# Optimization experiments

Hardware: AMD Instinct MI355X
Metric: run time of the kernel (lower is better)

Reference implementation:

```python
import jax, jax.numpy as jnp
import numpy as np
import math

B, N, D, H = 16, 1024, 1024, 8
HD = D // H
SCALE = 1.0 / math.sqrt(D // 8)
NEG = -1e30


def setup_inputs() -> dict:
    key = jax.random.key(0)
    ks = jax.random.split(key, 10)
    s = 0.02
    return {
        "x": jax.random.normal(ks[0], (B, N, D), dtype=jnp.float32),
        "x_mask": jax.random.randint(ks[1], (B, N), 0, 2, dtype=jnp.int32),
        "Wq": jax.random.normal(ks[2], (H, D, HD), dtype=jnp.float32) * s,
        "bq": jnp.zeros((H, HD), dtype=jnp.float32),
        "Wk": jax.random.normal(ks[3], (H, D, HD), dtype=jnp.float32) * s,
        "bk": jnp.zeros((H, HD), dtype=jnp.float32),
        "Wv": jax.random.normal(ks[4], (H, D, HD), dtype=jnp.float32) * s,
        "bv": jnp.zeros((H, HD), dtype=jnp.float32),
        "Wfc": jax.random.normal(ks[5], (D, D), dtype=jnp.float32) * s,
        "bfc": jnp.zeros((D,), dtype=jnp.float32),
    }


def reference(x, x_mask, Wq, bq, Wk, bk, Wv, bv, Wfc, bfc):
    # per-head projections, stacked: [B, H, N, HD]
    q = jnp.einsum("bnd,hde->bhne", x, Wq) + bq[None, :, None, :]
    k = jnp.einsum("bnd,hde->bhne", x, Wk) + bk[None, :, None, :]
    v = jnp.einsum("bnd,hde->bhne", x, Wv) + bv[None, :, None, :]
    # pairwise padding mask: mask & mask^T  ->  outer product for 0/1 values
    m = x_mask.astype(x.dtype)  # [B, N]
    mask = m[:, :, None] * m[:, None, :]  # [B, N, N]
    scores = jnp.einsum("bhne,bhme->bhnm", q, k) * SCALE  # [B, H, N, N]
    scores = scores * mask[:, None] + NEG * (1.0 - mask[:, None])
    attn = jax.nn.softmax(scores, axis=-1)
    o = jnp.einsum("bhnm,bhme->bhne", attn, v)  # [B, H, N, HD]
    # concat heads along feature dim (head order preserved)
    o = jnp.transpose(o, (0, 2, 1, 3)).reshape(B, N, D)
    out = o @ Wfc + bfc  # final fc; F.dropout result is discarded in source
    return out
```

## Files before the change

kernel.cpp:

```cpp
#include <hip/hip_runtime.h>
#include <hip/hip_bf16.h>
#include <math.h>

#define BN 1024
#define DD 1024
#define NB 16
#define NH 8
#define HDIM 128

typedef __attribute__((ext_vector_type(8))) short bf16x8;
typedef __attribute__((ext_vector_type(4))) float f32x4;
typedef __attribute__((ext_vector_type(16))) float f32x16;
typedef __attribute__((ext_vector_type(4))) unsigned short ushort4v;

#define DEV __device__ __forceinline__

DEV unsigned short f2bf(float f) {
  unsigned u = __float_as_uint(f);
  u = (u + 0x7fffu + ((u >> 16) & 1u)) >> 16;
  return (unsigned short)u;
}

DEV f32x4 mfma16(bf16x8 a, bf16x8 b, f32x4 c) {
  return __builtin_amdgcn_mfma_f32_16x16x32_bf16(a, b, c, 0, 0, 0);
}

DEV f32x16 mfma32(bf16x8 a, bf16x8 b, f32x16 c) {
  return __builtin_amdgcn_mfma_f32_32x32x16_bf16(a, b, c, 0, 0, 0);
}

DEV void async16(const unsigned short* g, unsigned short* l) {
  __builtin_amdgcn_global_load_lds(
      (const __attribute__((address_space(1))) unsigned short*)g,
      (__attribute__((address_space(3))) unsigned short*)l, 16, 0, 0);
}

DEV unsigned cvtpk(float lo, float hi_) {
  unsigned r;
  asm("v_cvt_pk_bf16_f32 %0, %1, %2" : "=v"(r) : "v"(lo), "v"(hi_));
  return r;
}
DEV void swap32(unsigned& a, unsigned& b) {
  asm volatile("v_permlane32_swap_b32 %0, %1" : "+v"(a), "+v"(b));
}
DEV bf16x8 mk8(unsigned a, unsigned b, unsigned c, unsigned d) {
  union { unsigned u[4]; bf16x8 v; } t;
  t.u[0] = a; t.u[1] = b; t.u[2] = c; t.u[3] = d;
  return t.v;
}

__global__ __launch_bounds__(256) void prep_kernel(
    const float* __restrict__ x, const float* __restrict__ Wq,
    const float* __restrict__ Wk, const float* __restrict__ Wv,
    const float* __restrict__ Wfc, unsigned short* __restrict__ x_bf,
    unsigned short* __restrict__ wqkvT, unsigned short* __restrict__ wfcT) {
  __shared__ float tile[32][33];
  const int bx = blockIdx.x, tid = threadIdx.x;
  if (bx < 16384) {
    int i = bx * 256 + tid;
    const float4* p = (const float4*)x;
    float4 v = p[i];
    ushort4v o;
    o[0] = f2bf(v.x); o[1] = f2bf(v.y); o[2] = f2bf(v.z); o[3] = f2bf(v.w);
    *(ushort4v*)(x_bf + (size_t)i * 4) = o;
    return;
  }
  const int tx = tid & 31, ty = tid >> 5;
  if (bx < 19456) {
    int idx = bx - 16384;
    int k0 = (idx & 31) * 32, e0 = ((idx >> 5) & 3) * 32, z = idx >> 7;
    int which = z >> 3, h = z & 7;
    const float* in = (which == 0 ? Wq : (which == 1 ? Wk : Wv)) + (size_t)h * DD * HDIM;
#pragma unroll
    for (int i = 0; i < 4; ++i)
      tile[ty + i * 8][tx] = in[(size_t)(k0 + ty + i * 8) * HDIM + e0 + tx];
    __syncthreads();
    int rowbase = which * 1024 + h * 128 + e0;
#pragma unroll
    for (int i = 0; i < 4; ++i)
      wqkvT[(size_t)(rowbase + ty + i * 8) * DD + k0 + tx] = f2bf(tile[tx][ty + i * 8]);
  } else {
    int idx = bx - 19456;
    int d0 = (idx & 31) * 32, c0 = (idx >> 5) * 32;
#pragma unroll
    for (int i = 0; i < 4; ++i)
      tile[ty + i * 8][tx] = Wfc[(size_t)(d0 + ty + i * 8) * DD + c0 + tx];
    __syncthreads();
#pragma unroll
    for (int i = 0; i < 4; ++i)
      wfcT[(size_t)(c0 + ty + i * 8) * DD + d0 + tx] = f2bf(tile[tx][ty + i * 8]);
  }
}

template <int MODE>
__global__ __launch_bounds__(256, 3) void gemm128_kernel(
    const unsigned short* __restrict__ A, const unsigned short* __restrict__ Bt,
    const float* __restrict__ bias0, const float* __restrict__ bias1,
    const float* __restrict__ bias2, unsigned short* __restrict__ out0,
    unsigned short* __restrict__ out1, unsigned short* __restrict__ out2,
    float* __restrict__ outf) {
  __shared__ unsigned short as[128 * 64];
  __shared__ unsigned short bs[128 * 64];
  const int tid = threadIdx.x;
  const int wave = tid >> 6, lane = tid & 63, quad = lane >> 4, l15 = lane & 15;
  const int wr = wave >> 1, wc = wave & 1;
  const int m0 = (blockIdx.x & 127) << 7, n0 = (blockIdx.x >> 7) << 7;
  f32x4 acc[4][4] = {};

  const int srow = wave * 32 + (lane >> 3);
  const int gch = ((lane & 7) - (lane >> 3)) & 7;
  const unsigned short* ag = A + (size_t)(m0 + srow) * 1024 + gch * 8;
  const unsigned short* bg = Bt + (size_t)(n0 + srow) * 1024 + gch * 8;
  unsigned short* as_w = as + wave * 32 * 64;
  unsigned short* bs_w = bs + wave * 32 * 64;

  for (int kb = 0; kb < 1024; kb += 64) {
#pragma unroll
    for (int i = 0; i < 4; ++i) {
      async16(ag + kb + i * 8 * 1024, as_w + i * 512);
      async16(bg + kb + i * 8 * 1024, bs_w + i * 512);
    }
    __syncthreads();
#pragma unroll
    for (int ks = 0; ks < 2; ++ks) {
      const int sl = ((quad + ks * 4 + l15) & 7) * 8;
      bf16x8 af[4], bfr[4];
#pragma unroll
      for (int mt = 0; mt < 4; ++mt)
        af[mt] = *(const bf16x8*)(as + (wr * 64 + mt * 16 + l15) * 64 + sl);
#pragma unroll
      for (int nt = 0; nt < 4; ++nt)
        bfr[nt] = *(const bf16x8*)(bs + (wc * 64 + nt * 16 + l15) * 64 + sl);
#pragma unroll
      for (int mt = 0; mt < 4; ++mt)
#pragma unroll
        for (int nt = 0; nt < 4; ++nt)
          acc[mt][nt] = mfma16(af[mt], bfr[nt], acc[mt][nt]);
    }
    __syncthreads();
  }

  if constexpr (MODE == 0) {
    const int seg = n0 >> 10;
#pragma unroll
    for (int mt = 0; mt < 4; ++mt) {
      int mb = m0 + wr * 64 + mt * 16 + quad * 4;
      int bb = mb >> 10, nn = mb & 1023;
#pragma unroll
      for (int nt = 0; nt < 4; ++nt) {
        int c = n0 + wc * 64 + nt * 16 + l15;
        int cc = c & 1023;
        int h = cc >> 7, e = cc & 127;
        if (seg == 2) {
          float bias = bias2[cc];
          ushort4v pv;
#pragma unroll
          for (int r = 0; r < 4; ++r) pv[r] = f2bf(acc[mt][nt][r] + bias);
          *(ushort4v*)(out2 + ((size_t)(bb * NH + h) * HDIM + e) * BN + nn) = pv;
        } else {
          const float* bp = (seg == 0) ? bias0 : bias1;
          unsigned short* op = (seg == 0) ? out0 : out1;
          float bias = bp[cc];
#pragma unroll
          for (int r = 0; r < 4; ++r)
            op[(((size_t)bb * NH + h) * BN + (nn + r)) * HDIM + e] =
                f2bf(acc[mt][nt][r] + bias);
        }
      }
    }
  } else {
#pragma unroll
    for (int mt = 0; mt < 4; ++mt) {
      int mb = m0 + wr * 64 + mt * 16 + quad * 4;
#pragma unroll
      for (int nt = 0; nt < 4; ++nt) {
        int c = n0 + wc * 64 + nt * 16 + l15;
        float bias = bias0[c];
#pragma unroll
        for (int r = 0; r < 4; ++r)
          outf[(size_t)(mb + r) * DD + c] = acc[mt][nt][r] + bias;
      }
    }
  }
}

__global__ __launch_bounds__(256, 2) void flash_attn_kernel(
    const unsigned short* __restrict__ Q, const unsigned short* __restrict__ Kk,
    const unsigned short* __restrict__ Vt, const int* __restrict__ xmask,
    unsigned short* __restrict__ O) {
  __shared__ unsigned short k_s[64 * 128];
  __shared__ unsigned short v_s[2][128 * 64];
  __shared__ float l_s[128];

  const float CL2E = 0.08838834764831845f * 1.44269504088896f;

  const int tid = threadIdx.x;
  const int w = tid >> 6, lane = tid & 63;
  const int l31 = lane & 31, hi = lane >> 5;
  const int lin = blockIdx.x;
  const int bh = lin & 127, qb = lin >> 7;
  const int b = bh >> 3, h = bh & 7;
  const int q0 = qb * 128;
  const unsigned short* qp = Q + ((size_t)bh * BN + q0) * HDIM;
  const unsigned short* kp = Kk + (size_t)bh * BN * HDIM;
  const unsigned short* vp = Vt + (size_t)bh * HDIM * BN;
  const int* xm_b = xmask + b * BN;

  bf16x8 qf[8];
#pragma unroll
  for (int dk = 0; dk < 8; ++dk)
    qf[dk] = *(const bf16x8*)(qp + (size_t)(w * 32 + l31) * HDIM + dk * 16 + hi * 8);

  const int rm = xm_b[q0 + w * 32 + l31];

  const int krow = lane >> 4;
  const int vrow = lane >> 3;
  const int vch = ((lane & 7) - vrow) & 7;

  float l_lane = 0.0f;
  f32x16 o_acc[4] = {};

#pragma unroll
  for (int i = 0; i < 4; ++i) {
    int rmod = i * 4 + krow;
    int g = ((lane & 15) - rmod) & 15;
    async16(kp + (size_t)(w * 16 + rmod) * HDIM + g * 8, k_s + (w * 16 + i * 4) * 128);
    int e = w * 32 + i * 8 + vrow;
    async16(vp + (size_t)e * BN + vch * 8, v_s[0] + (w * 32 + i * 8) * 64);
  }

  for (int it = 0; it < 16; ++it) {
    const int kb = it * 64;
    const unsigned long long mb = __ballot(xm_b[kb + lane] != 0);
    const unsigned long long mbh = mb >> (4 * hi);

    __syncthreads();

    f32x16 s0 = {}, s1 = {};
#pragma unroll
    for (int dk = 0; dk < 8; ++dk) {
      const int cc = (2 * dk + hi + (l31 & 15)) & 15;
      bf16x8 k0 = *(const bf16x8*)(k_s + (size_t)l31 * 128 + cc * 8);
      bf16x8 k1 = *(const bf16x8*)(k_s + (size_t)(32 + l31) * 128 + cc * 8);
      s0 = mfma32(k0, qf[dk], s0);
      s1 = mfma32(k1, qf[dk], s1);
    }

    float p0[16], p1[16];
#pragma unroll
    for (int r = 0; r < 16; ++r) {
      const int sh = (r & 3) + 8 * (r >> 2);
      float x0 = s0[r] * CL2E, x1 = s1[r] * CL2E;
      float t0 = ((mbh >> sh) & 1) ? x0 : -60.0f;
      float t1 = ((mbh >> (sh + 32)) & 1) ? x1 : -60.0f;
      float e0 = rm ? t0 : 0.0f;
      float e1 = rm ? t1 : 0.0f;
      p0[r] = __builtin_amdgcn_exp2f(e0);
      p1[r] = __builtin_amdgcn_exp2f(e1);
      l_lane += p0[r] + p1[r];
    }

    bf16x8 pa0, pa1, pa2, pa3;
    {
      unsigned a0 = cvtpk(p0[0], p0[1]), a1 = cvtpk(p0[2], p0[3]);
      unsigned a2 = cvtpk(p0[4], p0[5]), a3 = cvtpk(p0[6], p0[7]);
      unsigned b0 = cvtpk(p0[8], p0[9]), b1 = cvtpk(p0[10], p0[11]);
      unsigned b2 = cvtpk(p0[12], p0[13]), b3 = cvtpk(p0[14], p0[15]);
      swap32(a0, a2); swap32(a1, a3); swap32(b0, b2); swap32(b1, b3);
      pa0 = mk8(a0, a1, a2, a3);
      pa1 = mk8(b0, b1, b2, b3);
      unsigned c0 = cvtpk(p1[0], p1[1]), c1 = cvtpk(p1[2], p1[3]);
      unsigned c2 = cvtpk(p1[4], p1[5]), c3 = cvtpk(p1[6], p1[7]);
      unsigned d0 = cvtpk(p1[8], p1[9]), d1 = cvtpk(p1[10], p1[11]);
      unsigned d2 = cvtpk(p1[12], p1[13]), d3 = cvtpk(p1[14], p1[15]);
      swap32(c0, c2); swap32(c1, c3); swap32(d0, d2); swap32(d1, d3);
      pa2 = mk8(c0, c1, c2, c3);
      pa3 = mk8(d0, d1, d2, d3);
    }

    __syncthreads();

    {
      const int kn = (kb + 64) & (BN - 1);
      unsigned short* vb_next = v_s[(it + 1) & 1];
#pragma unroll
      for (int i = 0; i < 4; ++i) {
        int rmod = i * 4 + krow;
        int g = ((lane & 15) - rmod) & 15;
        async16(kp + (size_t)(kn + w * 16 + rmod) * HDIM + g * 8,
                k_s + (w * 16 + i * 4) * 128);
        int e = w * 32 + i * 8 + vrow;
        async16(vp + (size_t)e * BN + kn + vch * 8, vb_next + (w * 32 + i * 8) * 64);
      }
    }

    const unsigned short* vb = v_s[it & 1];
    __builtin_amdgcn_s_setprio(1);
#pragma unroll
    for (int et = 0; et < 4; ++et) {
      const int row = et * 32 + l31;
      const int cb = (hi + (row & 7)) & 7;
      bf16x8 v0 = *(const bf16x8*)(vb + (size_t)row * 64 + ((cb + 0) & 7) * 8);
      bf16x8 v1 = *(const bf16x8*)(vb + (size_t)row * 64 + ((cb + 2) & 7) * 8);
      bf16x8 v2 = *(const bf16x8*)(vb + (size_t)row * 64 + ((cb + 4) & 7) * 8);
      bf16x8 v3 = *(const bf16x8*)(vb + (size_t)row * 64 + ((cb + 6) & 7) * 8);
      o_acc[et] = mfma32(pa0, v0, o_acc[et]);
      o_acc[et] = mfma32(pa1, v1, o_acc[et]);
      o_acc[et] = mfma32(pa2, v2, o_acc[et]);
      o_acc[et] = mfma32(pa3, v3, o_acc[et]);
    }
    __builtin_amdgcn_s_setprio(0);
  }

  l_lane += __shfl_xor(l_lane, 32, 64);
  if (hi == 0) l_s[w * 32 + l31] = l_lane;
  __syncthreads();

#pragma unroll
  for (int r = 0; r < 16; ++r) {
    const int ql = (r & 3) + 8 * (r >> 2) + 4 * hi;
    const float inv = 1.0f / l_s[w * 32 + ql];
    const int row = q0 + w * 32 + ql;
#pragma unroll
    for (int et = 0; et < 4; ++et) {
      const int col = h * HDIM + et * 32 + l31;
      O[((size_t)b * BN + row) * DD + col] = f2bf(o_acc[et][r] * inv);
    }
  }
}

extern "C" void kernel_launch(void* const* d_in, const int* in_sizes, int n_in,
                              void* d_out, int out_size, void* d_ws, size_t ws_size,
                              hipStream_t stream) {
  const float* x = (const float*)d_in[0];
  const int* xmask = (const int*)d_in[1];
  const float* Wq = (const float*)d_in[2];
  const float* bq = (const float*)d_in[3];
  const float* Wk = (const float*)d_in[4];
  const float* bk = (const float*)d_in[5];
  const float* Wv = (const float*)d_in[6];
  const float* bv = (const float*)d_in[7];
  const float* Wfc = (const float*)d_in[8];
  const float* bfc = (const float*)d_in[9];
  float* out = (float*)d_out;

  char* ws = (char*)d_ws;
  unsigned short* x_bf  = (unsigned short*)(ws);
  unsigned short* wqkvT = (unsigned short*)(ws + 33554432);
  unsigned short* wfcT  = (unsigned short*)(ws + 39845888);
  unsigned short* q_bf  = (unsigned short*)(ws + 41943040);
  unsigned short* k_bf  = (unsigned short*)(ws + 75497472);
  unsigned short* vT_bf = (unsigned short*)(ws + 109051904);
  unsigned short* o_bf  = (unsigned short*)(ws + 142606336);

  prep_kernel<<<dim3(20480), dim3(256), 0, stream>>>(x, Wq, Wk, Wv, Wfc, x_bf, wqkvT, wfcT);

  gemm128_kernel<0><<<dim3(3072), dim3(256), 0, stream>>>(
      x_bf, wqkvT, bq, bk, bv, q_bf, k_bf, vT_bf, nullptr);

  flash_attn_kernel<<<dim3(1024), dim3(256), 0, stream>>>(q_bf, k_bf, vT_bf, xmask, o_bf);

  gemm128_kernel<1><<<dim3(1024), dim3(256), 0, stream>>>(
      o_bf, wfcT, bfc, nullptr, nullptr, nullptr, nullptr, nullptr, out);
}
```

Baseline: 395.0 us.

## Double-buffer K tile, drop mid-loop barrier, interleave softmax halves with PV MFMAs

K shared memory becomes double-buffered like V, so the next K/V tile prefetch is issued right after the single per-iteration barrier and the second __syncthreads is removed. The softmax exponentiation is split into two halves, each followed immediately by its share of the PV MFMAs, so exp/VALU work on one half can overlap matrix work on the other. This costs an extra 16KB of LDS per block, which may reduce occupancy under launch_bounds(256,2), and it relies on the async copy wait being handled correctly at the single barrier.

New measurement: 394.2 us. Within noise of the previous version (-0.2%).

```diff
diff --git a/kernel.cpp b/kernel.cpp
--- a/kernel.cpp
+++ b/kernel.cpp
@@ -188,7 +188,7 @@
     const unsigned short* __restrict__ Q, const unsigned short* __restrict__ Kk,
     const unsigned short* __restrict__ Vt, const int* __restrict__ xmask,
     unsigned short* __restrict__ O) {
-  __shared__ unsigned short k_s[64 * 128];
+  __shared__ unsigned short k_s[2][64 * 128];
   __shared__ unsigned short v_s[2][128 * 64];
   __shared__ float l_s[128];
 
@@ -224,92 +224,108 @@
   for (int i = 0; i < 4; ++i) {
     int rmod = i * 4 + krow;
     int g = ((lane & 15) - rmod) & 15;
-    async16(kp + (size_t)(w * 16 + rmod) * HDIM + g * 8, k_s + (w * 16 + i * 4) * 128);
+    async16(kp + (size_t)(w * 16 + rmod) * HDIM + g * 8, k_s[0] + (w * 16 + i * 4) * 128);
     int e = w * 32 + i * 8 + vrow;
     async16(vp + (size_t)e * BN + vch * 8, v_s[0] + (w * 32 + i * 8) * 64);
   }
 
   for (int it = 0; it < 16; ++it) {
     const int kb = it * 64;
+    const int cur = it & 1, nxt = cur ^ 1;
     const unsigned long long mb = __ballot(xm_b[kb + lane] != 0);
     const unsigned long long mbh = mb >> (4 * hi);
 
     __syncthreads();
 
+    {
+      const int kn = (kb + 64) & (BN - 1);
+      unsigned short* kbn = k_s[nxt];
+      unsigned short* vbn = v_s[nxt];
+#pragma unroll
+      for (int i = 0; i < 4; ++i) {
+        int rmod = i * 4 + krow;
+        int g = ((lane & 15) - rmod) & 15;
+        async16(kp + (size_t)(kn + w * 16 + rmod) * HDIM + g * 8,
+                kbn + (w * 16 + i * 4) * 128);
+        int e = w * 32 + i * 8 + vrow;
+        async16(vp + (size_t)e * BN + kn + vch * 8, vbn + (w * 32 + i * 8) * 64);
+      }
+    }
+
+    const unsigned short* kbc = k_s[cur];
     f32x16 s0 = {}, s1 = {};
 #pragma unroll
     for (int dk = 0; dk < 8; ++dk) {
       const int cc = (2 * dk + hi + (l31 & 15)) & 15;
-      bf16x8 k0 = *(const bf16x8*)(k_s + (size_t)l31 * 128 + cc * 8);
-      bf16x8 k1 = *(const bf16x8*)(k_s + (size_t)(32 + l31) * 128 + cc * 8);
+      bf16x8 k0 = *(const bf16x8*)(kbc + (size_t)l31 * 128 + cc * 8);
+      bf16x8 k1 = *(const bf16x8*)(kbc + (size_t)(32 + l31) * 128 + cc * 8);
       s0 = mfma32(k0, qf[dk], s0);
       s1 = mfma32(k1, qf[dk], s1);
     }
 
-    float p0[16], p1[16];
-#pragma unroll
-    for (int r = 0; r < 16; ++r) {
-      const int sh = (r & 3) + 8 * (r >> 2);
-      float x0 = s0[r] * CL2E, x1 = s1[r] * CL2E;
-      float t0 = ((mbh >> sh) & 1) ? x0 : -60.0f;
-      float t1 = ((mbh >> (sh + 32)) & 1) ? x1 : -60.0f;
-      float e0 = rm ? t0 : 0.0f;
-      float e1 = rm ? t1 : 0.0f;
-      p0[r] = __builtin_amdgcn_exp2f(e0);
-      p1[r] = __builtin_amdgcn_exp2f(e1);
-      l_lane += p0[r] + p1[r];
-    }
-
-    bf16x8 pa0, pa1, pa2, pa3;
+    const unsigned short* vb = v_s[cur];
+
     {
+      float p0[16];
+#pragma unroll
+      for (int r = 0; r < 16; ++r) {
+        const int sh = (r & 3) + 8 * (r >> 2);
+        float x0 = s0[r] * CL2E;
+        float t0 = ((mbh >> sh) & 1) ? x0 : -60.0f;
+        float e0 = rm ? t0 : 0.0f;
+        p0[r] = __builtin_amdgcn_exp2f(e0);
+        l_lane += p0[r];
+      }
       unsigned a0 = cvtpk(p0[0], p0[1]), a1 = cvtpk(p0[2], p0[3]);
       unsigned a2 = cvtpk(p0[4], p0[5]), a3 = cvtpk(p0[6], p0[7]);
       unsigned b0 = cvtpk(p0[8], p0[9]), b1 = cvtpk(p0[10], p0[11]);
       unsigned b2 = cvtpk(p0[12], p0[13]), b3 = cvtpk(p0[14], p0[15]);
       swap32(a0, a2); swap32(a1, a3); swap32(b0, b2); swap32(b1, b3);
-      pa0 = mk8(a0, a1, a2, a3);
-      pa1 = mk8(b0, b1, b2, b3);
+      bf16x8 pa0 = mk8(a0, a1, a2, a3);
+      bf16x8 pa1 = mk8(b0, b1, b2, b3);
+      __builtin_amdgcn_s_setprio(1);
+#pragma unroll
+      for (int et = 0; et < 4; ++et) {
+        const int row = et * 32 + l31;
+        const int cb = (hi + (row & 7)) & 7;
+        bf16x8 v0 = *(const bf16x8*)(vb + (size_t)row * 64 + ((cb + 0) & 7) * 8);
+        bf16x8 v1 = *(const bf16x8*)(vb + (size_t)row * 64 + ((cb + 2) & 7) * 8);
+        o_acc[et] = mfma32(pa0, v0, o_acc[et]);
+        o_acc[et] = mfma32(pa1, v1, o_acc[et]);
+      }
+      __builtin_amdgcn_s_setprio(0);
+    }
+
+    {
+      float p1[16];
+#pragma unroll
+      for (int r = 0; r < 16; ++r) {
+        const int sh = (r & 3) + 8 * (r >> 2);
+        float x1 = s1[r] * CL2E;
+        float t1 = ((mbh >> (sh + 32)) & 1) ? x1 : -60.0f;
+        float e1 = rm ? t1 : 0.0f;
+        p1[r] = __builtin_amdgcn_exp2f(e1);
+        l_lane += p1[r];
+      }
       unsigned c0 = cvtpk(p1[0], p1[1]), c1 = cvtpk(p1[2], p1[3]);
       unsigned c2 = cvtpk(p1[4], p1[5]), c3 = cvtpk(p1[6], p1[7]);
       unsigned d0 = cvtpk(p1[8], p1[9]), d1 = cvtpk(p1[10], p1[11]);
       unsigned d2 = cvtpk(p1[12], p1[13]), d3 = cvtpk(p1[14], p1[15]);
       swap32(c0, c2); swap32(c1, c3); swap32(d0, d2); swap32(d1, d3);
-      pa2 = mk8(c0, c1, c2, c3);
-      pa3 = mk8(d0, d1, d2, d3);
-    }
-
-    __syncthreads();
-
-    {
-      const int kn = (kb + 64) & (BN - 1);
-      unsigned short* vb_next = v_s[(it + 1) & 1];
-#pragma unroll
-      for (int i = 0; i < 4; ++i) {
-        int rmod = i * 4 + krow;
-        int g = ((lane & 15) - rmod) & 15;
-        async16(kp + (size_t)(kn + w * 16 + rmod) * HDIM + g * 8,
-                k_s + (w * 16 + i * 4) * 128);
-        int e = w * 32 + i * 8 + vrow;
-        async16(vp + (size_t)e * BN + kn + vch * 8, vb_next + (w * 32 + i * 8) * 64);
-      }
-    }
-
-    const unsigned short* vb = v_s[it & 1];
-    __builtin_amdgcn_s_setprio(1);
-#pragma unroll
-    for (int et = 0; et < 4; ++et) {
-      const int row = et * 32 + l31;
-      const int cb = (hi + (row & 7)) & 7;
-      bf16x8 v0 = *(const bf16x8*)(vb + (size_t)row * 64 + ((cb + 0) & 7) * 8);
-      bf16x8 v1 = *(const bf16x8*)(vb + (size_t)row * 64 + ((cb + 2) & 7) * 8);
-      bf16x8 v2 = *(const bf16x8*)(vb + (size_t)row * 64 + ((cb + 4) & 7) * 8);
-      bf16x8 v3 = *(const bf16x8*)(vb + (size_t)row * 64 + ((cb + 6) & 7) * 8);
-      o_acc[et] = mfma32(pa0, v0, o_acc[et]);
-      o_acc[et] = mfma32(pa1, v1, o_acc[et]);
-      o_acc[et] = mfma32(pa2, v2, o_acc[et]);
-      o_acc[et] = mfma32(pa3, v3, o_acc[et]);
-    }
-    __builtin_amdgcn_s_setprio(0);
+      bf16x8 pa2 = mk8(c0, c1, c2, c3);
+      bf16x8 pa3 = mk8(d0, d1, d2, d3);
+      __builtin_amdgcn_s_setprio(1);
+#pragma unroll
+      for (int et = 0; et < 4; ++et) {
+        const int row = et * 32 + l31;
+        const int cb = (hi + (row & 7)) & 7;
+        bf16x8 v2 = *(const bf16x8*)(vb + (size_t)row * 64 + ((cb + 4) & 7) * 8);
+        bf16x8 v3 = *(const bf16x8*)(vb + (size_t)row * 64 + ((cb + 6) & 7) * 8);
+        o_acc[et] = mfma32(pa2, v2, o_acc[et]);
+        o_acc[et] = mfma32(pa3, v3, o_acc[et]);
+      }
+      __builtin_amdgcn_s_setprio(0);
+    }
   }
 
   l_lane += __shfl_xor(l_lane, 32, 64);
```
